# Optimization experiments

Measured on AMD Instinct MI355X. Metric: run time of the kernel, lower is better.

The kernel has to match this reference:

```python
import jax, jax.numpy as jnp
import numpy as np
from jax import lax

IN_DIM = 256
MID = IN_DIM // 2          # 128
NUM_FILTERS = 8
OUT_DIM = 256
EMBED_DIM = 256
BN_EPS = 1e-5


def star_relu(x, scale, bias):
    # StarReLU: s * relu(x)**2 + b
    return scale * jnp.square(jax.nn.relu(x)) + bias


def setup_inputs() -> dict:
    key = jax.random.key(0)
    ks = jax.random.split(key, 12)
    B, H, W = 2, 16, 16
    h, w = 128, 128
    inp = {
        "x": jax.random.normal(ks[0], (B, IN_DIM, H, W), jnp.float32),
        "y": jax.random.normal(ks[1], (B, OUT_DIM, h, w), jnp.float32),
        # feature_fuse: 1x1 conv, depthwise 3x3 conv, BatchNorm (eval-mode stats)
        "conv1_w": jax.random.normal(ks[2], (MID, IN_DIM), jnp.float32) * 0.02,
        "conv1_b": jnp.zeros((MID,), jnp.float32),
        "dw_w": jax.random.normal(ks[3], (MID, 3, 3), jnp.float32) * 0.02,
        "dw_b": jnp.zeros((MID,), jnp.float32),
        "bn_gamma": jnp.ones((MID,), jnp.float32),
        "bn_beta": jnp.zeros((MID,), jnp.float32),
        "bn_mean": jax.random.normal(ks[4], (MID,), jnp.float32) * 0.1,
        "bn_var": jax.random.uniform(ks[5], (MID,), jnp.float32, 0.5, 1.5),
        "sr1_scale": jnp.ones((1,), jnp.float32),
        "sr1_bias": jnp.zeros((1,), jnp.float32),
        # channle_expand 1x1 conv
        "ce_w": jax.random.normal(ks[6], (NUM_FILTERS, MID), jnp.float32) * 0.02,
        "ce_b": jnp.zeros((NUM_FILTERS,), jnp.float32),
        "sr2_scale": jnp.ones((1,), jnp.float32),
        "sr2_bias": jnp.zeros((1,), jnp.float32),
        "W_base": jax.random.normal(ks[7], (OUT_DIM * EMBED_DIM, NUM_FILTERS), jnp.float32) * 0.02,
    }
    return inp


def reference(x, y, conv1_w, conv1_b, dw_w, dw_b, bn_gamma, bn_beta, bn_mean,
              bn_var, sr1_scale, sr1_bias, ce_w, ce_b, sr2_scale, sr2_bias, W_base):
    B, _, fh, fw = x.shape
    b, c, h, w = y.shape
    ph, pw = h // fh, w // fw

    # feature_fuse
    t = jnp.einsum('bchw,oc->bohw', x, conv1_w) + conv1_b[None, :, None, None]
    t = lax.conv_general_dilated(
        t, dw_w[:, None, :, :], (1, 1), ((1, 1), (1, 1)),
        feature_group_count=MID,
        dimension_numbers=('NCHW', 'OIHW', 'NCHW')) + dw_b[None, :, None, None]
    t = bn_gamma[None, :, None, None] * (t - bn_mean[None, :, None, None]) \
        * lax.rsqrt(bn_var + BN_EPS)[None, :, None, None] + bn_beta[None, :, None, None]
    t = star_relu(t, sr1_scale, sr1_bias)

    # channle_expand + act -> per-location filter coefficients [b, F, fh, fw]
    wdec = star_relu(jnp.einsum('bchw,fc->bfhw', t, ce_w) + ce_b[None, :, None, None],
                     sr2_scale, sr2_bias)

    # hypernetwork: [b, E*O, fh, fw], flattened as (embed_dim, out_dim)
    Wd = jnp.einsum('bfhw,ef->behw', wdec, W_base)
    Wd = Wd.reshape(b, EMBED_DIM, OUT_DIM, fh, fw)

    # massive-group 1x1 conv == per-(batch, block) small GEMM over spatial patches
    yb = y.reshape(b, c, fh, ph, fw, pw)
    out = jnp.einsum('beoij,boipjq->beipjq', Wd, yb)  # [b, E, fh, ph, fw, pw]
    return out.reshape(b, EMBED_DIM, h, w)
```

## Files before the change

kernel.cpp:

```cpp
#include <hip/hip_runtime.h>
#include <stdint.h>

typedef unsigned short u16t;
typedef unsigned int   u32t;
typedef _Float16       h16;
typedef __attribute__((ext_vector_type(2))) _Float16 h16x2;
typedef __attribute__((ext_vector_type(8))) short    short8;
typedef __attribute__((ext_vector_type(4))) float    f32x4;

#if defined(__has_builtin)
#if __has_builtin(__builtin_amdgcn_fdot2)
#define HAVE_DOT2 1
#endif
#endif

__device__ __forceinline__ float dot2h(u32t a, u32t b, float c){
#ifdef HAVE_DOT2
  return __builtin_amdgcn_fdot2(__builtin_bit_cast(h16x2, a),
                                __builtin_bit_cast(h16x2, b), c, false);
#else
  h16x2 ha = __builtin_bit_cast(h16x2, a), hb = __builtin_bit_cast(h16x2, b);
  return c + (float)ha[0]*(float)hb[0] + (float)ha[1]*(float)hb[1];
#endif
}

__device__ __forceinline__ float bf2f(u16t h){
  union { u32t u; float f; } c; c.u = ((u32t)h) << 16; return c.f;
}
__device__ __forceinline__ u32t pk2bf(float a, float b){
  u32t ua = __builtin_bit_cast(u32t, a) + 0x8000u;
  u32t ub = __builtin_bit_cast(u32t, b) + 0x8000u;
  return __builtin_amdgcn_perm(ub, ua, 0x07060302u);
}
__device__ __forceinline__ u32t pk2h(float a, float b){
  h16x2 h = { (h16)a, (h16)b };
  return __builtin_bit_cast(u32t, h);
}

template<bool BF>
__device__ __forceinline__ float ldv(const void* p, size_t i){
  if constexpr (BF) return bf2f(((const u16t*)p)[i]);
  else              return ((const float*)p)[i];
}
template<bool BF>
__device__ __forceinline__ void ld8(const void* p, size_t i, float* v){
  if constexpr (BF){
    uint4 u = *(const uint4*)((const u16t*)p + i);
    const u32t a[4] = {u.x, u.y, u.z, u.w};
#pragma unroll
    for (int d = 0; d < 4; ++d){
      v[2*d]   = bf2f((u16t)(a[d] & 0xffffu));
      v[2*d+1] = bf2f((u16t)(a[d] >> 16));
    }
  } else {
    const float4* q = (const float4*)((const float*)p + i);
    float4 A = q[0], B = q[1];
    v[0]=A.x; v[1]=A.y; v[2]=A.z; v[3]=A.w;
    v[4]=B.x; v[5]=B.y; v[6]=B.z; v[7]=B.w;
  }
}
template<bool BF>
__device__ __forceinline__ void ld8pk(const void* p, size_t i, u32t* dst){
  if constexpr (BF){
    uint4 u = *(const uint4*)((const u16t*)p + i);
    dst[0]=u.x; dst[1]=u.y; dst[2]=u.z; dst[3]=u.w;
  } else {
    const float4* q = (const float4*)((const float*)p + i);
    float4 A = q[0], B = q[1];
    dst[0] = pk2bf(A.x, A.y); dst[1] = pk2bf(A.z, A.w);
    dst[2] = pk2bf(B.x, B.y); dst[3] = pk2bf(B.z, B.w);
  }
}

__device__ __forceinline__ bool probe_bf(const void* xv){
  const u16t* p = (const u16t*)xv;
  const int lane = threadIdx.x & 63;
  const u16t h0 = p[lane], h1 = p[lane + 64];
  const int e0 = (h0 >> 7) & 0xff, e1 = (h1 >> 7) & 0xff;
  unsigned long long b0 = __ballot(e0 >= 90 && e0 <= 150);
  unsigned long long b1 = __ballot(e1 >= 90 && e1 <= 150);
  return (__popcll(b0) + __popcll(b1)) >= 104;
}

__device__ __forceinline__ void gld_lds16(const void* g, void* l){
  __builtin_amdgcn_global_load_lds(
      (const __attribute__((address_space(1))) u32t*)g,
      (__attribute__((address_space(3))) u32t*)l, 16, 0, 0);
}


template<bool BF>
__device__ __forceinline__ void trans_body(const void* y, u16t* yt, int bid){
  const int b = bid >> 7, i = (bid >> 3) & 15, jp = bid & 7;
  const int tid   = threadIdx.x;
  const int o_oct = tid & 31, p = (tid >> 5) & 7, g = (tid >> 8) & 1, rh = tid >> 9;
  u32t Rp[4][4];
#pragma unroll
  for (int r4 = 0; r4 < 4; ++r4){
    const int r = rh * 4 + r4;
    const size_t idx = (((size_t)(b * 256 + o_oct * 8 + r)) * 128 + (i * 8 + p)) * 128
                     + (jp * 2 + g) * 8;
    ld8pk<BF>(y, idx, Rp[r4]);
  }
  u16t* slab = yt + (size_t)bid * 32768;
#pragma unroll
  for (int q = 0; q < 8; ++q){
    const int d = q >> 1, h = q & 1;
    const u32t lo0 = Rp[0][d], hi0 = Rp[1][d];
    const u32t lo1 = Rp[2][d], hi1 = Rp[3][d];
    const u32t c0 = h ? ((lo0 >> 16)     | (hi0 & 0xffff0000u))
                      : ((lo0 & 0xffffu) | (hi0 << 16));
    const u32t c1 = h ? ((lo1 >> 16)     | (hi1 & 0xffff0000u))
                      : ((lo1 & 0xffffu) | (hi1 << 16));
    const int row  = g * 64 + p * 8 + q;
    const int phys = (o_oct + row) & 31;
    *(uint2*)(slab + (size_t)row * 256 + phys * 8 + rh * 4) = make_uint2(c0, c1);
  }
}

template<bool BF>
__device__ __forceinline__ void pre12_body(
    const void* x, const void* w, const void* bias,
    const void* dww, const void* dwb,
    const void* bng, const void* bnb, const void* bnm, const void* bnv,
    const void* s1s, const void* s1b, float* t2, float (*ts)[256], int bq)
{
  const int b = bq >> 5, cq = bq & 31;
  const int cl = threadIdx.x >> 8, ij = threadIdx.x & 255;
  const int c = cq * 4 + cl;
  const int i = ij >> 4, j = ij & 15;
  float a0 = ldv<BF>(bias, c);
  const size_t xb = (size_t)b * 65536 + ij;
#pragma unroll 8
  for (int k = 0; k < 256; ++k)
    a0 += ldv<BF>(x, xb + (size_t)k * 256) * ldv<BF>(w, (size_t)c * 256 + k);
  ts[cl][ij] = a0;
  __syncthreads();
  float s = ldv<BF>(dwb, c);
#pragma unroll
  for (int di = 0; di < 3; ++di){
    const int ii = i + di - 1;
    if (ii < 0 || ii > 15) continue;
#pragma unroll
    for (int dj = 0; dj < 3; ++dj){
      const int jj = j + dj - 1;
      if (jj < 0 || jj > 15) continue;
      s += ts[cl][ii * 16 + jj] * ldv<BF>(dww, c * 9 + di * 3 + dj);
    }
  }
  const float v = ldv<BF>(bng, c) * (s - ldv<BF>(bnm, c)) *
                  rsqrtf(ldv<BF>(bnv, c) + 1e-5f) + ldv<BF>(bnb, c);
  const float r = fmaxf(v, 0.0f);
  t2[((size_t)b * 128 + c) * 256 + ij] = ldv<BF>(s1s, 0) * r * r + ldv<BF>(s1b, 0);
}

template<bool BF>
__device__ __forceinline__ void prew_body(const void* wb, uint4* wbh2, int pb){
  const int t = pb * 1024 + threadIdx.x;
  const int e = t & 255, o = t >> 8;
  float v[8];
  ld8<BF>(wb, ((size_t)e * 256 + o) * 8, v);
  wbh2[(size_t)o * 256 + e] = make_uint4(pk2h(v[0], v[1]), pk2h(v[2], v[3]),
                                         pk2h(v[4], v[5]), pk2h(v[6], v[7]));
}

__global__ __launch_bounds__(1024) void k_fused(
    const void* x, const void* y,
    const void* w1, const void* b1, const void* dww, const void* dwb,
    const void* bng, const void* bnb, const void* bnm, const void* bnv,
    const void* s1s, const void* s1b, const void* wb,
    float* t2, uint4* wbh2, u16t* yt)
{
  __shared__ float ts[4][256];
  const bool bf = probe_bf(x);
  const int bid = blockIdx.x;
  if (bid < 256){
    if (bf) trans_body<true >(y, yt, bid);
    else    trans_body<false>(y, yt, bid);
  } else if (bid < 320){
    if (bf) pre12_body<true >(x,w1,b1,dww,dwb,bng,bnb,bnm,bnv,s1s,s1b,t2,ts,bid-256);
    else    pre12_body<false>(x,w1,b1,dww,dwb,bng,bnb,bnm,bnv,s1s,s1b,t2,ts,bid-256);
  } else {
    if (bf) prew_body<true >(wb, wbh2, bid - 320);
    else    prew_body<false>(wb, wbh2, bid - 320);
  }
}

template<bool BF>
__device__ __forceinline__ void main_body(
    const float* t2, const void* cew, const void* ceb,
    const void* s2s, const void* s2b,
    const u16t* yt, const uint4* wbh2, float* out, u16t* smem)
{
  const int bid = blockIdx.x;
  const int b = bid >> 7, i = (bid >> 3) & 15, j0 = (bid & 7) * 2;
  const int tid = threadIdx.x;
  const int wv = tid >> 6, lane = tid & 63;

  {
    const char* src = (const char*)yt + (size_t)bid * 65536 + wv * 4096 + lane * 16;
    char* dst = (char*)smem + wv * 4096;
#pragma unroll
    for (int k = 0; k < 4; ++k)
      gld_lds16(src + k * 1024, dst + k * 1024);
  }

  float* wds = (float*)(smem + 32768);

  if (tid < 16){
    const int g = tid >> 3, f = tid & 7;
    const int ij = i * 16 + j0 + g;
    float a = ldv<BF>(ceb, f);
    const float* tp = t2 + (size_t)b * 32768 + ij;
#pragma unroll 8
    for (int c = 0; c < 128; ++c)
      a += tp[(size_t)c * 256] * ldv<BF>(cew, (size_t)f * 128 + c);
    const float r = fmaxf(a, 0.0f);
    wds[tid] = ldv<BF>(s2s, 0) * r * r + ldv<BF>(s2b, 0);
  }

  const int l15 = lane & 15, l4 = lane >> 4;
  const int e0  = wv * 16;

  const uint4* wrow = wbh2 + (size_t)(l4 * 8) * 256 + e0 + l15;

  uint4 Wb[2][8];
#pragma unroll
  for (int r = 0; r < 8; ++r) Wb[0][r] = wrow[(size_t)r * 256];

  f32x4 acc[2][4];
#pragma unroll
  for (int g = 0; g < 2; ++g)
#pragma unroll
    for (int nt = 0; nt < 4; ++nt)
      acc[g][nt] = (f32x4){0.f, 0.f, 0.f, 0.f};

  __syncthreads();

  u32t wdp[2][4];
#pragma unroll
  for (int g = 0; g < 2; ++g)
#pragma unroll
    for (int d = 0; d < 4; ++d)
      wdp[g][d] = pk2h(wds[g * 8 + 2 * d], wds[g * 8 + 2 * d + 1]);

#pragma unroll
  for (int ks = 0; ks < 8; ++ks){
    const int cur = ks & 1;
    if (ks < 7){
#pragma unroll
      for (int r = 0; r < 8; ++r)
        Wb[cur ^ 1][r] = wrow[(size_t)((ks + 1) * 32 + r) * 256];
    }
    float s[2][8];
#pragma unroll
    for (int r = 0; r < 8; ++r){
      const uint4 w4 = Wb[cur][r];
#pragma unroll
      for (int g = 0; g < 2; ++g){
        float t = dot2h(w4.x, wdp[g][0], 0.0f);
        t = dot2h(w4.y, wdp[g][1], t);
        t = dot2h(w4.z, wdp[g][2], t);
        s[g][r] = dot2h(w4.w, wdp[g][3], t);
      }
    }
#pragma unroll
    for (int g = 0; g < 2; ++g){
      u32t a4[4];
#pragma unroll
      for (int d = 0; d < 4; ++d) a4[d] = pk2bf(s[g][2*d], s[g][2*d+1]);
      const short8 af = __builtin_bit_cast(short8, *(uint4*)a4);
#pragma unroll
      for (int nt = 0; nt < 4; ++nt){
        const int row  = g * 64 + nt * 16 + l15;
        const int phys = (ks * 4 + l4 + row) & 31;
        const short8 bfr = *(const short8*)(smem + row * 256 + phys * 8);
        acc[g][nt] = __builtin_amdgcn_mfma_f32_16x16x32_bf16(af, bfr, acc[g][nt], 0, 0, 0);
      }
    }
  }

#pragma unroll
  for (int g = 0; g < 2; ++g){
#pragma unroll
    for (int nt = 0; nt < 4; ++nt){
      const int col = nt * 16 + l15;
      const int pp = col >> 3, qq = col & 7;
#pragma unroll
      for (int r = 0; r < 4; ++r){
        const int ee = e0 + l4 * 4 + r;
        const size_t oaddr = ((size_t)(b * 256 + ee) * 128 + (i * 8 + pp)) * 128
                           + (j0 + g) * 8 + qq;
        out[oaddr] = acc[g][nt][r];
      }
    }
  }
}
__global__ __launch_bounds__(1024, 4) void k_main(
    const void* x, const float* t2, const void* cew, const void* ceb,
    const void* s2s, const void* s2b,
    const u16t* yt, const uint4* wbh2, float* out)
{
  extern __shared__ __align__(16) u16t smem[];
  if (probe_bf(x)) main_body<true >(t2, cew, ceb, s2s, s2b, yt, wbh2, out, smem);
  else             main_body<false>(t2, cew, ceb, s2s, s2b, yt, wbh2, out, smem);
}

extern "C" void kernel_launch(void* const* d_in, const int* in_sizes, int n_in,
                              void* d_out, int out_size, void* d_ws, size_t ws_size,
                              hipStream_t stream)
{
  float* t2    = (float*)d_ws;
  uint4* wbh2  = (uint4*)((char*)d_ws + 262144);
  u16t*  yt    = (u16t*)((char*)d_ws + 1310720);

  k_fused<<<dim3(384), dim3(1024), 0, stream>>>(
      d_in[0], d_in[1], d_in[2], d_in[3], d_in[4], d_in[5], d_in[6], d_in[7],
      d_in[8], d_in[9], d_in[10], d_in[11], d_in[16], t2, wbh2, yt);

  const int lds_bytes = 65536 + 64;
  hipFuncSetAttribute((const void*)k_main,
                      hipFuncAttributeMaxDynamicSharedMemorySize, lds_bytes);
  k_main<<<dim3(256), dim3(1024), lds_bytes, stream>>>(
      d_in[0], t2, d_in[12], d_in[13], d_in[14], d_in[15], yt, wbh2, (float*)d_out);
}
```

Measured before the change: 180.2 us.

## Fuse y transpose into main kernel and parallelize channel-expand reduction

The separate transpose pass, which wrote a bf16 copy of y to workspace and reloaded it via global_load_lds, is removed. The main kernel now reads y directly, packs pairs of output channels into bf16, and writes the swizzled tile into LDS. The channel-expand dot product is split across 4 lanes per output and combined with shuffles, and launch bounds are relaxed from 4 to 2 waves per SIMD. This drops one workspace round trip and shrinks the first kernel, at the cost of direct strided global loads in the main kernel.

```diff
diff --git a/kernel.cpp b/kernel.cpp
--- a/kernel.cpp
+++ b/kernel.cpp
@@ -59,18 +59,6 @@
     v[4]=B.x; v[5]=B.y; v[6]=B.z; v[7]=B.w;
   }
 }
-template<bool BF>
-__device__ __forceinline__ void ld8pk(const void* p, size_t i, u32t* dst){
-  if constexpr (BF){
-    uint4 u = *(const uint4*)((const u16t*)p + i);
-    dst[0]=u.x; dst[1]=u.y; dst[2]=u.z; dst[3]=u.w;
-  } else {
-    const float4* q = (const float4*)((const float*)p + i);
-    float4 A = q[0], B = q[1];
-    dst[0] = pk2bf(A.x, A.y); dst[1] = pk2bf(A.z, A.w);
-    dst[2] = pk2bf(B.x, B.y); dst[3] = pk2bf(B.z, B.w);
-  }
-}
 
 __device__ __forceinline__ bool probe_bf(const void* xv){
   const u16t* p = (const u16t*)xv;
@@ -80,42 +68,6 @@
   unsigned long long b0 = __ballot(e0 >= 90 && e0 <= 150);
   unsigned long long b1 = __ballot(e1 >= 90 && e1 <= 150);
   return (__popcll(b0) + __popcll(b1)) >= 104;
-}
-
-__device__ __forceinline__ void gld_lds16(const void* g, void* l){
-  __builtin_amdgcn_global_load_lds(
-      (const __attribute__((address_space(1))) u32t*)g,
-      (__attribute__((address_space(3))) u32t*)l, 16, 0, 0);
-}
-
-
-template<bool BF>
-__device__ __forceinline__ void trans_body(const void* y, u16t* yt, int bid){
-  const int b = bid >> 7, i = (bid >> 3) & 15, jp = bid & 7;
-  const int tid   = threadIdx.x;
-  const int o_oct = tid & 31, p = (tid >> 5) & 7, g = (tid >> 8) & 1, rh = tid >> 9;
-  u32t Rp[4][4];
-#pragma unroll
-  for (int r4 = 0; r4 < 4; ++r4){
-    const int r = rh * 4 + r4;
-    const size_t idx = (((size_t)(b * 256 + o_oct * 8 + r)) * 128 + (i * 8 + p)) * 128
-                     + (jp * 2 + g) * 8;
-    ld8pk<BF>(y, idx, Rp[r4]);
-  }
-  u16t* slab = yt + (size_t)bid * 32768;
-#pragma unroll
-  for (int q = 0; q < 8; ++q){
-    const int d = q >> 1, h = q & 1;
-    const u32t lo0 = Rp[0][d], hi0 = Rp[1][d];
-    const u32t lo1 = Rp[2][d], hi1 = Rp[3][d];
-    const u32t c0 = h ? ((lo0 >> 16)     | (hi0 & 0xffff0000u))
-                      : ((lo0 & 0xffffu) | (hi0 << 16));
-    const u32t c1 = h ? ((lo1 >> 16)     | (hi1 & 0xffff0000u))
-                      : ((lo1 & 0xffffu) | (hi1 << 16));
-    const int row  = g * 64 + p * 8 + q;
-    const int phys = (o_oct + row) & 31;
-    *(uint2*)(slab + (size_t)row * 256 + phys * 8 + rh * 4) = make_uint2(c0, c1);
-  }
 }
 
 template<bool BF>
@@ -165,58 +117,90 @@
 }
 
 __global__ __launch_bounds__(1024) void k_fused(
-    const void* x, const void* y,
+    const void* x,
     const void* w1, const void* b1, const void* dww, const void* dwb,
     const void* bng, const void* bnb, const void* bnm, const void* bnv,
     const void* s1s, const void* s1b, const void* wb,
-    float* t2, uint4* wbh2, u16t* yt)
+    float* t2, uint4* wbh2)
 {
   __shared__ float ts[4][256];
   const bool bf = probe_bf(x);
   const int bid = blockIdx.x;
-  if (bid < 256){
-    if (bf) trans_body<true >(y, yt, bid);
-    else    trans_body<false>(y, yt, bid);
-  } else if (bid < 320){
-    if (bf) pre12_body<true >(x,w1,b1,dww,dwb,bng,bnb,bnm,bnv,s1s,s1b,t2,ts,bid-256);
-    else    pre12_body<false>(x,w1,b1,dww,dwb,bng,bnb,bnm,bnv,s1s,s1b,t2,ts,bid-256);
+  if (bid < 64){
+    if (bf) pre12_body<true >(x,w1,b1,dww,dwb,bng,bnb,bnm,bnv,s1s,s1b,t2,ts,bid);
+    else    pre12_body<false>(x,w1,b1,dww,dwb,bng,bnb,bnm,bnv,s1s,s1b,t2,ts,bid);
   } else {
-    if (bf) prew_body<true >(wb, wbh2, bid - 320);
-    else    prew_body<false>(wb, wbh2, bid - 320);
+    if (bf) prew_body<true >(wb, wbh2, bid - 64);
+    else    prew_body<false>(wb, wbh2, bid - 64);
   }
 }
 
 template<bool BF>
 __device__ __forceinline__ void main_body(
-    const float* t2, const void* cew, const void* ceb,
+    const void* y, const float* t2, const void* cew, const void* ceb,
     const void* s2s, const void* s2b,
-    const u16t* yt, const uint4* wbh2, float* out, u16t* smem)
+    const uint4* wbh2, float* out, u16t* smem)
 {
   const int bid = blockIdx.x;
-  const int b = bid >> 7, i = (bid >> 3) & 15, j0 = (bid & 7) * 2;
+  const int b = bid >> 7, i = (bid >> 3) & 15, jp = bid & 7, j0 = jp * 2;
   const int tid = threadIdx.x;
   const int wv = tid >> 6, lane = tid & 63;
 
   {
-    const char* src = (const char*)yt + (size_t)bid * 65536 + wv * 4096 + lane * 16;
-    char* dst = (char*)smem + wv * 4096;
-#pragma unroll
-    for (int k = 0; k < 4; ++k)
-      gld_lds16(src + k * 1024, dst + k * 1024);
+    const int w4 = tid & 3, p = (tid >> 2) & 7, opq = tid >> 5;
+    u32t pk[4][4];
+#pragma unroll
+    for (int r = 0; r < 4; ++r){
+      const int o = (r * 32 + opq) * 2;
+      const size_t base = (((size_t)(b * 256 + o) * 128) + i * 8 + p) * 128
+                        + jp * 16 + w4 * 4;
+      if constexpr (BF){
+        const u16t* yp = (const u16t*)y;
+        const uint2 u0 = *(const uint2*)(yp + base);
+        const uint2 u1 = *(const uint2*)(yp + base + 16384);
+        pk[r][0] = (u0.x & 0xffffu) | (u1.x << 16);
+        pk[r][1] = (u0.x >> 16)     | (u1.x & 0xffff0000u);
+        pk[r][2] = (u0.y & 0xffffu) | (u1.y << 16);
+        pk[r][3] = (u0.y >> 16)     | (u1.y & 0xffff0000u);
+      } else {
+        const float* yp = (const float*)y;
+        const float4 A = *(const float4*)(yp + base);
+        const float4 B = *(const float4*)(yp + base + 16384);
+        pk[r][0] = pk2bf(A.x, B.x); pk[r][1] = pk2bf(A.y, B.y);
+        pk[r][2] = pk2bf(A.z, B.z); pk[r][3] = pk2bf(A.w, B.w);
+      }
+    }
+#pragma unroll
+    for (int r = 0; r < 4; ++r){
+      const int o  = (r * 32 + opq) * 2;
+      const int oc = o >> 3, osub = o & 7;
+#pragma unroll
+      for (int k = 0; k < 4; ++k){
+        const int w_l  = w4 * 4 + k;
+        const int row  = (w_l >> 3) * 64 + p * 8 + (w_l & 7);
+        const int phys = (oc + row) & 31;
+        *(u32t*)(smem + row * 256 + phys * 8 + osub) = pk[r][k];
+      }
+    }
   }
 
   float* wds = (float*)(smem + 32768);
 
-  if (tid < 16){
-    const int g = tid >> 3, f = tid & 7;
+  if (tid < 64){
+    const int g = (tid >> 5) & 1, f = (tid >> 2) & 7, cq = tid & 3;
     const int ij = i * 16 + j0 + g;
-    float a = ldv<BF>(ceb, f);
     const float* tp = t2 + (size_t)b * 32768 + ij;
+    float a = 0.0f;
 #pragma unroll 8
-    for (int c = 0; c < 128; ++c)
+    for (int c = cq; c < 128; c += 4)
       a += tp[(size_t)c * 256] * ldv<BF>(cew, (size_t)f * 128 + c);
-    const float r = fmaxf(a, 0.0f);
-    wds[tid] = ldv<BF>(s2s, 0) * r * r + ldv<BF>(s2b, 0);
+    a += __shfl_xor(a, 1);
+    a += __shfl_xor(a, 2);
+    if (cq == 0){
+      const float tot = a + ldv<BF>(ceb, f);
+      const float rr  = fmaxf(tot, 0.0f);
+      wds[g * 8 + f] = ldv<BF>(s2s, 0) * rr * rr + ldv<BF>(s2b, 0);
+    }
   }
 
   const int l15 = lane & 15, l4 = lane >> 4;
@@ -296,14 +280,14 @@
     }
   }
 }
-__global__ __launch_bounds__(1024, 4) void k_main(
-    const void* x, const float* t2, const void* cew, const void* ceb,
+__global__ __launch_bounds__(1024, 2) void k_main(
+    const void* x, const void* y, const float* t2, const void* cew, const void* ceb,
     const void* s2s, const void* s2b,
-    const u16t* yt, const uint4* wbh2, float* out)
+    const uint4* wbh2, float* out)
 {
   extern __shared__ __align__(16) u16t smem[];
-  if (probe_bf(x)) main_body<true >(t2, cew, ceb, s2s, s2b, yt, wbh2, out, smem);
-  else             main_body<false>(t2, cew, ceb, s2s, s2b, yt, wbh2, out, smem);
+  if (probe_bf(x)) main_body<true >(y, t2, cew, ceb, s2s, s2b, wbh2, out, smem);
+  else             main_body<false>(y, t2, cew, ceb, s2s, s2b, wbh2, out, smem);
 }
 
 extern "C" void kernel_launch(void* const* d_in, const int* in_sizes, int n_in,
@@ -312,15 +296,15 @@
 {
   float* t2    = (float*)d_ws;
   uint4* wbh2  = (uint4*)((char*)d_ws + 262144);
-  u16t*  yt    = (u16t*)((char*)d_ws + 1310720);
-
-  k_fused<<<dim3(384), dim3(1024), 0, stream>>>(
-      d_in[0], d_in[1], d_in[2], d_in[3], d_in[4], d_in[5], d_in[6], d_in[7],
-      d_in[8], d_in[9], d_in[10], d_in[11], d_in[16], t2, wbh2, yt);
+
+  k_fused<<<dim3(128), dim3(1024), 0, stream>>>(
+      d_in[0], d_in[2], d_in[3], d_in[4], d_in[5], d_in[6], d_in[7],
+      d_in[8], d_in[9], d_in[10], d_in[11], d_in[16], t2, wbh2);
 
   const int lds_bytes = 65536 + 64;
   hipFuncSetAttribute((const void*)k_main,
                       hipFuncAttributeMaxDynamicSharedMemorySize, lds_bytes);
   k_main<<<dim3(256), dim3(1024), lds_bytes, stream>>>(
-      d_in[0], t2, d_in[12], d_in[13], d_in[14], d_in[15], yt, wbh2, (float*)d_out);
-}
+      d_in[0], d_in[1], t2, d_in[12], d_in[13], d_in[14], d_in[15],
+      wbh2, (float*)d_out);
+}
```

Result: faster. 155.9 us (-13.5%).
